# Kernel tuning notes

Measured on AMD Instinct MI355X. Metric: run time of the kernel, lower is better.

## Reference

```python
import jax, jax.numpy as jnp
import numpy as np

TEMPERATURE = 0.5
EPS = 1e-20


def setup_inputs() -> dict:
    key = jax.random.key(0)
    ks = jax.random.split(key, 7)
    N, T, S = 16, 64, 1024
    SRC, TGT, D = 512, 512, 64
    return {
        "input": jax.random.normal(ks[0], (N, T, TGT), jnp.float32),
        "memory_bank": jax.random.normal(ks[1], (N, S, SRC), jnp.float32),
        "W_q": jax.random.normal(ks[2], (TGT, D), jnp.float32) / np.sqrt(TGT),
        "W_ctx": jax.random.normal(ks[3], (SRC, D), jnp.float32) / np.sqrt(SRC),
        "v": jax.random.normal(ks[4], (D,), jnp.float32) / np.sqrt(D),
        "W_out": jax.random.normal(ks[5], (SRC + TGT, TGT), jnp.float32) / np.sqrt(SRC + TGT),
        "b_out": jax.random.normal(ks[6], (TGT,), jnp.float32) * 0.01,
    }


def reference(input, memory_bank, W_q, W_ctx, v, W_out, b_out):
    # MLP attention score: v^T tanh(W_q q + W_ctx h)
    wq = jnp.einsum("ntd,de->nte", input, W_q)            # [N,T,D]
    uh = jnp.einsum("nsd,de->nse", memory_bank, W_ctx)    # [N,S,D]
    wquh = jnp.tanh(wq[:, :, None, :] + uh[:, None, :, :])  # [N,T,S,D]
    scores = jnp.einsum("ntsd,d->nts", wquh, v)           # [N,T,S]

    log_alpha = jax.nn.log_softmax(scores, axis=-1)
    alpha = jnp.exp(log_alpha)                            # c_align_vectors

    # deterministic context + output
    context_c = jnp.einsum("nts,nsd->ntd", alpha, memory_bank)
    h_c = jnp.tanh(jnp.concatenate([input, context_c], axis=-1) @ W_out + b_out)

    # gumbel-softmax sample (K = n_samples = 1, forced by view_as in original)
    u = jax.random.uniform(jax.random.key(42), log_alpha.shape, jnp.float32)
    g = -jnp.log(-jnp.log(u + EPS) + EPS)                 # gumbel noise
    y_align = jax.nn.softmax((log_alpha + g) / TEMPERATURE, axis=-1)  # [N,T,S]

    context_y = jnp.einsum("nts,nsd->ntd", y_align, memory_bank)
    h_y = jnp.tanh(jnp.concatenate([input, context_y], axis=-1) @ W_out + b_out)

    return jnp.stack([h_c, h_y], axis=0)  # [2,N,T,tgt_dim]
```

## Files before the change

kernel.cpp:

```cpp
#include <hip/hip_runtime.h>
#include <hip/hip_bf16.h>
#include <stdint.h>

#define DEV __device__ __forceinline__

typedef __attribute__((ext_vector_type(8))) short short8;
typedef __attribute__((ext_vector_type(4))) float f32x4;

#define TWO_LOG2E 2.8853900817779268f

DEV unsigned short f2bf(float f) {
  uint32_t u = __float_as_uint(f);
  u += 0x7FFFu + ((u >> 16) & 1u);
  return (unsigned short)(u >> 16);
}

DEV uint2 pk4(float4 f) {
  union { __hip_bfloat162 h; unsigned u; } a, b;
  a.h = __float22bfloat162_rn(make_float2(f.x, f.y));
  b.h = __float22bfloat162_rn(make_float2(f.z, f.w));
  return make_uint2(a.u, b.u);
}

DEV short8 mk8(uint2 lo, uint2 hi) {
  union { short8 s; uint4 u; } t;
  t.u = make_uint4(lo.x, lo.y, hi.x, hi.y);
  return t.s;
}

DEV uint32_t rotl32(uint32_t x, int r) { return (x << r) | (x >> (32 - r)); }

DEV void threefry_0_42(uint32_t x0, uint32_t x1, uint32_t& o0, uint32_t& o1) {
  const uint32_t ks0 = 0u, ks1 = 42u, ks2 = 0x1BD11BDAu ^ 42u;
  x0 += ks0; x1 += ks1;
#define TFR(r) { x0 += x1; x1 = rotl32(x1, (r)); x1 ^= x0; }
  TFR(13) TFR(15) TFR(26) TFR(6)  x0 += ks1; x1 += ks2 + 1u;
  TFR(17) TFR(29) TFR(16) TFR(24) x0 += ks2; x1 += ks0 + 2u;
  TFR(13) TFR(15) TFR(26) TFR(6)  x0 += ks0; x1 += ks1 + 3u;
  TFR(17) TFR(29) TFR(16) TFR(24) x0 += ks1; x1 += ks2 + 4u;
  TFR(13) TFR(15) TFR(26) TFR(6)  x0 += ks2; x1 += ks0 + 5u;
#undef TFR
  o0 = x0; o1 = x1;
}

DEV float wredmax(float v) {
#pragma unroll
  for (int off = 32; off > 0; off >>= 1) v = fmaxf(v, __shfl_xor(v, off));
  return v;
}
DEV float wredsum(float v) {
#pragma unroll
  for (int off = 32; off > 0; off >>= 1) v += __shfl_xor(v, off);
  return v;
}

__global__ __launch_bounds__(256) void transpose_all(const float* __restrict__ Wctx,
                                                     const float* __restrict__ Wq,
                                                     const float* __restrict__ Wout,
                                                     unsigned short* __restrict__ WctxT,
                                                     unsigned short* __restrict__ WqT,
                                                     unsigned short* __restrict__ WoutT) {
  __shared__ float tile[64][65];
  const int b = blockIdx.x;
  const float* src; unsigned short* dst; int R, C, br, bc;
  if (b < 8)       { src = Wctx; dst = WctxT; R = 512;  C = 64;  br = b * 64;        bc = 0; }
  else if (b < 16) { src = Wq;   dst = WqT;   R = 512;  C = 64;  br = (b - 8) * 64;  bc = 0; }
  else { int i = b - 16; src = Wout; dst = WoutT; R = 1024; C = 512; br = (i & 15) * 64; bc = (i >> 4) * 64; }
  const int tid = threadIdx.x;
  const int lr = tid >> 4, lc4 = (tid & 15) * 4;
#pragma unroll
  for (int i = 0; i < 4; ++i) {
    float4 v = *(const float4*)(src + (long)(br + lr + i * 16) * C + bc + lc4);
    tile[lr + i * 16][lc4 + 0] = v.x;
    tile[lr + i * 16][lc4 + 1] = v.y;
    tile[lr + i * 16][lc4 + 2] = v.z;
    tile[lr + i * 16][lc4 + 3] = v.w;
  }
  __syncthreads();
#pragma unroll
  for (int i = 0; i < 4; ++i) {
    int crow = lr + i * 16;
    ushort4 o;
    o.x = f2bf(tile[lc4 + 0][crow]);
    o.y = f2bf(tile[lc4 + 1][crow]);
    o.z = f2bf(tile[lc4 + 2][crow]);
    o.w = f2bf(tile[lc4 + 3][crow]);
    *(ushort4*)(dst + (long)(bc + crow) * R + br + lc4) = o;
  }
}

__global__ __launch_bounds__(256) void gemm_uhwq(const float* __restrict__ mb,
                                                 const float* __restrict__ input,
                                                 const unsigned short* __restrict__ WctxT,
                                                 const unsigned short* __restrict__ WqT,
                                                 float* __restrict__ uhT,
                                                 float* __restrict__ wqo) {
  __shared__ unsigned short As[64][32];
  __shared__ unsigned short Bs[64][32];
  const int tid = threadIdx.x;
  const int bx = blockIdx.x;
  const float* A;  const unsigned short* BT;  int mbase;
  if (bx < 256) { A = mb;    BT = WctxT; mbase = bx * 64; }
  else          { A = input; BT = WqT;   mbase = (bx - 256) * 64; }
  const int srow = tid >> 2, kc = tid & 3;
  const int scol = ((kc ^ (srow & 3)) * 8);
  const int wave = tid >> 6, lane = tid & 63;
  const int wm = (wave >> 1) * 32, wn = (wave & 1) * 32;
  const int q = lane >> 4, r = lane & 15;
  const int c0 = ((q ^ (r & 3)) * 8);
  const float* ap = A + (long)(mbase + srow) * 512 + kc * 8;
  const unsigned short* bp = BT + (long)srow * 512 + kc * 8;
  f32x4 acc[2][2];
#pragma unroll
  for (int i = 0; i < 2; ++i)
#pragma unroll
    for (int j = 0; j < 2; ++j) acc[i][j] = (f32x4){0.f, 0.f, 0.f, 0.f};

  float4 fa0 = *(const float4*)(ap);
  float4 fa1 = *(const float4*)(ap + 4);
  uint4 fb = *(const uint4*)(bp);
  for (int k0 = 0; k0 < 512; k0 += 32) {
    uint2 p0 = pk4(fa0), p1 = pk4(fa1);
    *(uint4*)&As[srow][scol] = make_uint4(p0.x, p0.y, p1.x, p1.y);
    *(uint4*)&Bs[srow][scol] = fb;
    __syncthreads();
    if (k0 + 32 < 512) {
      fa0 = *(const float4*)(ap + k0 + 32);
      fa1 = *(const float4*)(ap + k0 + 36);
      fb = *(const uint4*)(bp + k0 + 32);
    }
    short8 a0 = *(const short8*)&As[wm + r][c0];
    short8 a1 = *(const short8*)&As[wm + 16 + r][c0];
    short8 b0 = *(const short8*)&Bs[wn + r][c0];
    short8 b1 = *(const short8*)&Bs[wn + 16 + r][c0];
    acc[0][0] = __builtin_amdgcn_mfma_f32_16x16x32_bf16(a0, b0, acc[0][0], 0, 0, 0);
    acc[0][1] = __builtin_amdgcn_mfma_f32_16x16x32_bf16(a0, b1, acc[0][1], 0, 0, 0);
    acc[1][0] = __builtin_amdgcn_mfma_f32_16x16x32_bf16(a1, b0, acc[1][0], 0, 0, 0);
    acc[1][1] = __builtin_amdgcn_mfma_f32_16x16x32_bf16(a1, b1, acc[1][1], 0, 0, 0);
    __syncthreads();
  }
#pragma unroll
  for (int i2 = 0; i2 < 2; ++i2)
#pragma unroll
    for (int j2 = 0; j2 < 2; ++j2) {
      int gcol = wn + j2 * 16 + r;
      int m = mbase + wm + i2 * 16 + q * 4;
      if (bx < 256) {
        int n = m >> 10, s0 = m & 1023;
        float4 o;
        o.x = acc[i2][j2][0] * TWO_LOG2E;
        o.y = acc[i2][j2][1] * TWO_LOG2E;
        o.z = acc[i2][j2][2] * TWO_LOG2E;
        o.w = acc[i2][j2][3] * TWO_LOG2E;
        *(float4*)(uhT + (long)n * 65536 + (long)gcol * 1024 + s0) = o;
      } else {
#pragma unroll
        for (int reg = 0; reg < 4; ++reg)
          wqo[(long)(m + reg) * 64 + gcol] = acc[i2][j2][reg] * TWO_LOG2E;
      }
    }
}

__global__ __launch_bounds__(256) void gemm_ctx_mfma(const float* __restrict__ alpha,
                                                     const float* __restrict__ yal,
                                                     const float* __restrict__ mb,
                                                     float* __restrict__ ctx) {
  __shared__ unsigned short As[64][32];
  const int tid = threadIdx.x;
  const int vt = blockIdx.x >> 4, n = blockIdx.x & 15;
  const int dbase = blockIdx.y * 32;
  const int srow = tid >> 2, kc = tid & 3;
  const int scol = ((kc ^ (srow & 3)) * 8);
  const int wave = tid >> 6, lane = tid & 63;
  const int wm = (wave >> 1) * 32, wn = (wave & 1) * 16;
  const int q = lane >> 4, r = lane & 15;
  const int c0 = ((q ^ (r & 3)) * 8);
  const float* Abase = (vt == 0 ? alpha : yal) + (long)n * 65536;
  const float* ap = Abase + (long)srow * 1024 + kc * 8;
  const float* bcol = mb + (long)n * 524288 + dbase + wn + r;
  f32x4 acc[2];
  acc[0] = (f32x4){0.f, 0.f, 0.f, 0.f};
  acc[1] = (f32x4){0.f, 0.f, 0.f, 0.f};

  float4 fa0 = *(const float4*)(ap);
  float4 fa1 = *(const float4*)(ap + 4);
  float bv[8];
#pragma unroll
  for (int j = 0; j < 8; ++j) bv[j] = bcol[(long)(q * 8 + j) * 512];

  for (int k0 = 0; k0 < 1024; k0 += 32) {
    uint2 p0 = pk4(fa0), p1 = pk4(fa1);
    *(uint4*)&As[srow][scol] = make_uint4(p0.x, p0.y, p1.x, p1.y);
    __syncthreads();
    float4 blo = make_float4(bv[0], bv[1], bv[2], bv[3]);
    float4 bhi = make_float4(bv[4], bv[5], bv[6], bv[7]);
    short8 b0 = mk8(pk4(blo), pk4(bhi));
    if (k0 + 32 < 1024) {
      fa0 = *(const float4*)(ap + k0 + 32);
      fa1 = *(const float4*)(ap + k0 + 36);
#pragma unroll
      for (int j = 0; j < 8; ++j) bv[j] = bcol[(long)(k0 + 32 + q * 8 + j) * 512];
    }
    short8 a0 = *(const short8*)&As[wm + r][c0];
    short8 a1 = *(const short8*)&As[wm + 16 + r][c0];
    acc[0] = __builtin_amdgcn_mfma_f32_16x16x32_bf16(a0, b0, acc[0], 0, 0, 0);
    acc[1] = __builtin_amdgcn_mfma_f32_16x16x32_bf16(a1, b0, acc[1], 0, 0, 0);
    __syncthreads();
  }
#pragma unroll
  for (int i2 = 0; i2 < 2; ++i2) {
    int gcol = dbase + wn + r;
#pragma unroll
    for (int reg = 0; reg < 4; ++reg) {
      long grow = (long)vt * 1024 + n * 64 + wm + i2 * 16 + q * 4 + reg;
      ctx[grow * 512 + gcol] = acc[i2][reg];
    }
  }
}

__global__ __launch_bounds__(256) void gemm_out_mfma(const float* __restrict__ input,
                                                     const float* __restrict__ ctx,
                                                     const unsigned short* __restrict__ WoutT,
                                                     const float* __restrict__ bout,
                                                     float* __restrict__ out) {
  __shared__ unsigned short As[64][32];
  __shared__ unsigned short Bs[32][32];
  const int tid = threadIdx.x;
  const int mbase = blockIdx.x * 64, nbase = blockIdx.y * 32;
  const int srow = tid >> 2, kc = tid & 3;
  const int scol = ((kc ^ (srow & 3)) * 8);
  const int wave = tid >> 6, lane = tid & 63;
  const int wm = (wave >> 1) * 32, wn = (wave & 1) * 16;
  const int q = lane >> 4, r = lane & 15;
  const int c0 = ((q ^ (r & 3)) * 8);
  const int vv = mbase >> 10, nt = (mbase + srow) & 1023;
  const float* ap_lo = input + (long)nt * 512 + kc * 8;
  const float* ap_hi = ctx + (long)(vv * 1024 + nt) * 512 + kc * 8 - 512;
  const int brow = (tid & 127) >> 2;
  const unsigned short* bp = WoutT + (long)(nbase + brow) * 1024 + kc * 8;
  f32x4 acc[2];
  acc[0] = (f32x4){0.f, 0.f, 0.f, 0.f};
  acc[1] = (f32x4){0.f, 0.f, 0.f, 0.f};

  float4 fa0 = *(const float4*)(ap_lo);
  float4 fa1 = *(const float4*)(ap_lo + 4);
  uint4 fb;
  if (tid < 128) fb = *(const uint4*)(bp);
  for (int k0 = 0; k0 < 1024; k0 += 32) {
    uint2 p0 = pk4(fa0), p1 = pk4(fa1);
    *(uint4*)&As[srow][scol] = make_uint4(p0.x, p0.y, p1.x, p1.y);
    if (tid < 128) *(uint4*)&Bs[brow][(kc ^ (brow & 3)) * 8] = fb;
    __syncthreads();
    int kn = k0 + 32;
    if (kn < 1024) {
      const float* apn = (kn < 512) ? ap_lo : ap_hi;
      fa0 = *(const float4*)(apn + kn);
      fa1 = *(const float4*)(apn + kn + 4);
      if (tid < 128) fb = *(const uint4*)(bp + kn);
    }
    short8 a0 = *(const short8*)&As[wm + r][c0];
    short8 a1 = *(const short8*)&As[wm + 16 + r][c0];
    short8 b0 = *(const short8*)&Bs[wn + r][c0];
    acc[0] = __builtin_amdgcn_mfma_f32_16x16x32_bf16(a0, b0, acc[0], 0, 0, 0);
    acc[1] = __builtin_amdgcn_mfma_f32_16x16x32_bf16(a1, b0, acc[1], 0, 0, 0);
    __syncthreads();
  }
#pragma unroll
  for (int i2 = 0; i2 < 2; ++i2) {
    int gcol = nbase + wn + r;
    float bb = bout[gcol];
#pragma unroll
    for (int reg = 0; reg < 4; ++reg) {
      int grow = mbase + wm + i2 * 16 + q * 4 + reg;
      float z = acc[i2][reg] + bb;
      float rc = __builtin_amdgcn_rcpf(1.f + __builtin_amdgcn_exp2f(z * TWO_LOG2E));
      out[(long)grow * 512 + gcol] = fmaf(-2.f, rc, 1.f);
    }
  }
}

__global__ __launch_bounds__(256) void scores_kernel(const float* __restrict__ uhT,
                                                     const float* __restrict__ wq2,
                                                     const float* __restrict__ v,
                                                     float* __restrict__ alpha_g,
                                                     float* __restrict__ y_g) {
  const int tid = threadIdx.x;
  const int nt = blockIdx.x;
  const int n = nt >> 6;
  __shared__ float wvs[64];
  __shared__ float vvs[64];
  __shared__ float red[4];
  if (tid < 64) {
    wvs[tid] = wq2[nt * 64 + tid];
    vvs[tid] = v[tid];
  }
  __syncthreads();

  float sumv = 0.f;
#pragma unroll
  for (int d = 0; d < 64; d += 4) {
    float4 vv = *(const float4*)&vvs[d];
    sumv += vv.x + vv.y + vv.z + vv.w;
  }

  const float* un = uhT + (long)n * 65536 + tid * 4;
  float4 racc = make_float4(0.f, 0.f, 0.f, 0.f);
  for (int db = 0; db < 64; db += 8) {
    float4 ub[8];
#pragma unroll
    for (int j = 0; j < 8; ++j) ub[j] = *(const float4*)(un + (long)(db + j) * 1024);
#pragma unroll
    for (int j = 0; j < 8; ++j) {
      float w = wvs[db + j], vvj = vvs[db + j];
      racc.x = fmaf(vvj, __builtin_amdgcn_rcpf(1.f + __builtin_amdgcn_exp2f(ub[j].x + w)), racc.x);
      racc.y = fmaf(vvj, __builtin_amdgcn_rcpf(1.f + __builtin_amdgcn_exp2f(ub[j].y + w)), racc.y);
      racc.z = fmaf(vvj, __builtin_amdgcn_rcpf(1.f + __builtin_amdgcn_exp2f(ub[j].z + w)), racc.z);
      racc.w = fmaf(vvj, __builtin_amdgcn_rcpf(1.f + __builtin_amdgcn_exp2f(ub[j].w + w)), racc.w);
    }
  }
  float lsc[4];
  lsc[0] = fmaf(-2.f, racc.x, sumv);
  lsc[1] = fmaf(-2.f, racc.y, sumv);
  lsc[2] = fmaf(-2.f, racc.z, sumv);
  lsc[3] = fmaf(-2.f, racc.w, sumv);

  const int wv = tid >> 6, ln = tid & 63;
  float m = fmaxf(fmaxf(lsc[0], lsc[1]), fmaxf(lsc[2], lsc[3]));
  m = wredmax(m);
  if (ln == 0) red[wv] = m;
  __syncthreads();
  m = fmaxf(fmaxf(red[0], red[1]), fmaxf(red[2], red[3]));
  __syncthreads();
  float ss = 0.f;
#pragma unroll
  for (int i = 0; i < 4; ++i) ss += __expf(lsc[i] - m);
  ss = wredsum(ss);
  if (ln == 0) red[wv] = ss;
  __syncthreads();
  ss = red[0] + red[1] + red[2] + red[3];
  const float logl = __logf(ss);
  __syncthreads();

  const uint32_t jbase = (uint32_t)nt * 1024u + (uint32_t)tid * 4u;
  float ys[4];
  float4 av;
#pragma unroll
  for (int i = 0; i < 4; ++i) {
    float la = lsc[i] - m - logl;
    ((float*)&av)[i] = __expf(la);
    uint32_t o0, o1;
    threefry_0_42(0u, jbase + i, o0, o1);
    uint32_t bits = o0 ^ o1;
    float u = __uint_as_float((bits >> 9) | 0x3f800000u) - 1.0f;
    float g = -__logf(-__logf(u + 1e-20f) + 1e-20f);
    ys[i] = (la + g) * 2.0f;
  }
  *(float4*)(alpha_g + (long)nt * 1024 + tid * 4) = av;

  float m2 = fmaxf(fmaxf(ys[0], ys[1]), fmaxf(ys[2], ys[3]));
  m2 = wredmax(m2);
  if (ln == 0) red[wv] = m2;
  __syncthreads();
  m2 = fmaxf(fmaxf(red[0], red[1]), fmaxf(red[2], red[3]));
  __syncthreads();
  float s2 = 0.f;
  float4 ye;
#pragma unroll
  for (int i = 0; i < 4; ++i) { ((float*)&ye)[i] = __expf(ys[i] - m2); s2 += ((float*)&ye)[i]; }
  s2 = wredsum(s2);
  if (ln == 0) red[wv] = s2;
  __syncthreads();
  s2 = red[0] + red[1] + red[2] + red[3];
  const float rinv = __fdividef(1.f, s2);
  ye.x *= rinv; ye.y *= rinv; ye.z *= rinv; ye.w *= rinv;
  *(float4*)(y_g + (long)nt * 1024 + tid * 4) = ye;
}

extern "C" void kernel_launch(void* const* d_in, const int* in_sizes, int n_in,
                              void* d_out, int out_size, void* d_ws, size_t ws_size,
                              hipStream_t stream) {
  const float* input = (const float*)d_in[0];
  const float* mb    = (const float*)d_in[1];
  const float* W_q   = (const float*)d_in[2];
  const float* W_ctx = (const float*)d_in[3];
  const float* v     = (const float*)d_in[4];
  const float* W_out = (const float*)d_in[5];
  const float* b_out = (const float*)d_in[6];
  float* out = (float*)d_out;
  float* ws = (float*)d_ws;

  float* uhT   = ws;
  float* wq    = ws + 1048576;
  float* yal   = ws + 1114112;
  unsigned short* WctxT = (unsigned short*)(ws + 2162688);
  unsigned short* WqT   = (unsigned short*)(ws + 2179072);
  unsigned short* WoutT = (unsigned short*)(ws + 2195456);
  float* alpha = out;
  float* ctx   = uhT;

  transpose_all<<<144, 256, 0, stream>>>(W_ctx, W_q, W_out, WctxT, WqT, WoutT);
  gemm_uhwq<<<272, 256, 0, stream>>>(mb, input, WctxT, WqT, uhT, wq);
  scores_kernel<<<1024, 256, 0, stream>>>(uhT, wq, v, alpha, yal);
  gemm_ctx_mfma<<<dim3(32, 16), 256, 0, stream>>>(alpha, yal, mb, ctx);
  gemm_out_mfma<<<dim3(32, 16), 256, 0, stream>>>(input, ctx, WoutT, b_out, out);
}
```

Baseline: 154.3 us.

## Split output GEMM into shared input part, store alpha/y/ctx as bf16, merge ctx blocks

The input half of the concatenated output projection is the same for both the deterministic and the sampled branch. It is now computed once into P, and the output GEMM only runs over the context half, starting from P. Alpha, the Gumbel weights and the context are written as bf16 instead of fp32, which halves intermediate traffic and removes the in-loop conversions. The context GEMM now uses 512-thread blocks that process alpha and y together, so each memory_bank tile is loaded once for both. This adds a launch and a P buffer and takes some precision loss from rounding the context to bf16.

```diff
diff --git a/kernel.cpp b/kernel.cpp
--- a/kernel.cpp
+++ b/kernel.cpp
@@ -161,68 +161,10 @@
     }
 }
 
-__global__ __launch_bounds__(256) void gemm_ctx_mfma(const float* __restrict__ alpha,
-                                                     const float* __restrict__ yal,
-                                                     const float* __restrict__ mb,
-                                                     float* __restrict__ ctx) {
-  __shared__ unsigned short As[64][32];
-  const int tid = threadIdx.x;
-  const int vt = blockIdx.x >> 4, n = blockIdx.x & 15;
-  const int dbase = blockIdx.y * 32;
-  const int srow = tid >> 2, kc = tid & 3;
-  const int scol = ((kc ^ (srow & 3)) * 8);
-  const int wave = tid >> 6, lane = tid & 63;
-  const int wm = (wave >> 1) * 32, wn = (wave & 1) * 16;
-  const int q = lane >> 4, r = lane & 15;
-  const int c0 = ((q ^ (r & 3)) * 8);
-  const float* Abase = (vt == 0 ? alpha : yal) + (long)n * 65536;
-  const float* ap = Abase + (long)srow * 1024 + kc * 8;
-  const float* bcol = mb + (long)n * 524288 + dbase + wn + r;
-  f32x4 acc[2];
-  acc[0] = (f32x4){0.f, 0.f, 0.f, 0.f};
-  acc[1] = (f32x4){0.f, 0.f, 0.f, 0.f};
-
-  float4 fa0 = *(const float4*)(ap);
-  float4 fa1 = *(const float4*)(ap + 4);
-  float bv[8];
-#pragma unroll
-  for (int j = 0; j < 8; ++j) bv[j] = bcol[(long)(q * 8 + j) * 512];
-
-  for (int k0 = 0; k0 < 1024; k0 += 32) {
-    uint2 p0 = pk4(fa0), p1 = pk4(fa1);
-    *(uint4*)&As[srow][scol] = make_uint4(p0.x, p0.y, p1.x, p1.y);
-    __syncthreads();
-    float4 blo = make_float4(bv[0], bv[1], bv[2], bv[3]);
-    float4 bhi = make_float4(bv[4], bv[5], bv[6], bv[7]);
-    short8 b0 = mk8(pk4(blo), pk4(bhi));
-    if (k0 + 32 < 1024) {
-      fa0 = *(const float4*)(ap + k0 + 32);
-      fa1 = *(const float4*)(ap + k0 + 36);
-#pragma unroll
-      for (int j = 0; j < 8; ++j) bv[j] = bcol[(long)(k0 + 32 + q * 8 + j) * 512];
-    }
-    short8 a0 = *(const short8*)&As[wm + r][c0];
-    short8 a1 = *(const short8*)&As[wm + 16 + r][c0];
-    acc[0] = __builtin_amdgcn_mfma_f32_16x16x32_bf16(a0, b0, acc[0], 0, 0, 0);
-    acc[1] = __builtin_amdgcn_mfma_f32_16x16x32_bf16(a1, b0, acc[1], 0, 0, 0);
-    __syncthreads();
-  }
-#pragma unroll
-  for (int i2 = 0; i2 < 2; ++i2) {
-    int gcol = dbase + wn + r;
-#pragma unroll
-    for (int reg = 0; reg < 4; ++reg) {
-      long grow = (long)vt * 1024 + n * 64 + wm + i2 * 16 + q * 4 + reg;
-      ctx[grow * 512 + gcol] = acc[i2][reg];
-    }
-  }
-}
-
-__global__ __launch_bounds__(256) void gemm_out_mfma(const float* __restrict__ input,
-                                                     const float* __restrict__ ctx,
-                                                     const unsigned short* __restrict__ WoutT,
-                                                     const float* __restrict__ bout,
-                                                     float* __restrict__ out) {
+__global__ __launch_bounds__(256) void gemm_pre(const float* __restrict__ input,
+                                                const unsigned short* __restrict__ WoutT,
+                                                const float* __restrict__ bout,
+                                                float* __restrict__ P) {
   __shared__ unsigned short As[64][32];
   __shared__ unsigned short Bs[32][32];
   const int tid = threadIdx.x;
@@ -233,29 +175,26 @@
   const int wm = (wave >> 1) * 32, wn = (wave & 1) * 16;
   const int q = lane >> 4, r = lane & 15;
   const int c0 = ((q ^ (r & 3)) * 8);
-  const int vv = mbase >> 10, nt = (mbase + srow) & 1023;
-  const float* ap_lo = input + (long)nt * 512 + kc * 8;
-  const float* ap_hi = ctx + (long)(vv * 1024 + nt) * 512 + kc * 8 - 512;
+  const float* ap = input + (long)(mbase + srow) * 512 + kc * 8;
   const int brow = (tid & 127) >> 2;
   const unsigned short* bp = WoutT + (long)(nbase + brow) * 1024 + kc * 8;
   f32x4 acc[2];
   acc[0] = (f32x4){0.f, 0.f, 0.f, 0.f};
   acc[1] = (f32x4){0.f, 0.f, 0.f, 0.f};
 
-  float4 fa0 = *(const float4*)(ap_lo);
-  float4 fa1 = *(const float4*)(ap_lo + 4);
+  float4 fa0 = *(const float4*)(ap);
+  float4 fa1 = *(const float4*)(ap + 4);
   uint4 fb;
   if (tid < 128) fb = *(const uint4*)(bp);
-  for (int k0 = 0; k0 < 1024; k0 += 32) {
+  for (int k0 = 0; k0 < 512; k0 += 32) {
     uint2 p0 = pk4(fa0), p1 = pk4(fa1);
     *(uint4*)&As[srow][scol] = make_uint4(p0.x, p0.y, p1.x, p1.y);
     if (tid < 128) *(uint4*)&Bs[brow][(kc ^ (brow & 3)) * 8] = fb;
     __syncthreads();
     int kn = k0 + 32;
-    if (kn < 1024) {
-      const float* apn = (kn < 512) ? ap_lo : ap_hi;
-      fa0 = *(const float4*)(apn + kn);
-      fa1 = *(const float4*)(apn + kn + 4);
+    if (kn < 512) {
+      fa0 = *(const float4*)(ap + kn);
+      fa1 = *(const float4*)(ap + kn + 4);
       if (tid < 128) fb = *(const uint4*)(bp + kn);
     }
     short8 a0 = *(const short8*)&As[wm + r][c0];
@@ -272,7 +211,118 @@
 #pragma unroll
     for (int reg = 0; reg < 4; ++reg) {
       int grow = mbase + wm + i2 * 16 + q * 4 + reg;
-      float z = acc[i2][reg] + bb;
+      P[(long)grow * 512 + gcol] = acc[i2][reg] + bb;
+    }
+  }
+}
+
+__global__ __launch_bounds__(512) void gemm_ctx_mfma(const unsigned short* __restrict__ alpha,
+                                                     const unsigned short* __restrict__ yal,
+                                                     const float* __restrict__ mb,
+                                                     unsigned short* __restrict__ ctx) {
+  __shared__ unsigned short As[2][64][32];
+  const int tid = threadIdx.x;
+  const int n = blockIdx.x, dbase = blockIdx.y * 32;
+  const int half = tid >> 8, st = tid & 255;
+  const int srow = st >> 2, kc = st & 3;
+  const int scol = ((kc ^ (srow & 3)) * 8);
+  const unsigned short* Ab = (half ? yal : alpha) + (long)n * 65536 + (long)srow * 1024 + kc * 8;
+  const int wave = tid >> 6, lane = tid & 63;
+  const int vt = wave >> 2, wm = ((wave >> 1) & 1) * 32, wn = (wave & 1) * 16;
+  const int q = lane >> 4, r = lane & 15;
+  const int c0 = ((q ^ (r & 3)) * 8);
+  const float* bcol = mb + (long)n * 524288 + dbase + wn + r;
+  f32x4 acc[2];
+  acc[0] = (f32x4){0.f, 0.f, 0.f, 0.f};
+  acc[1] = (f32x4){0.f, 0.f, 0.f, 0.f};
+
+  uint4 fa = *(const uint4*)(Ab);
+  float bv[8];
+#pragma unroll
+  for (int j = 0; j < 8; ++j) bv[j] = bcol[(long)(q * 8 + j) * 512];
+
+  for (int k0 = 0; k0 < 1024; k0 += 32) {
+    *(uint4*)&As[half][srow][scol] = fa;
+    __syncthreads();
+    float4 blo = make_float4(bv[0], bv[1], bv[2], bv[3]);
+    float4 bhi = make_float4(bv[4], bv[5], bv[6], bv[7]);
+    short8 b0 = mk8(pk4(blo), pk4(bhi));
+    if (k0 + 32 < 1024) {
+      fa = *(const uint4*)(Ab + k0 + 32);
+#pragma unroll
+      for (int j = 0; j < 8; ++j) bv[j] = bcol[(long)(k0 + 32 + q * 8 + j) * 512];
+    }
+    short8 a0 = *(const short8*)&As[vt][wm + r][c0];
+    short8 a1 = *(const short8*)&As[vt][wm + 16 + r][c0];
+    acc[0] = __builtin_amdgcn_mfma_f32_16x16x32_bf16(a0, b0, acc[0], 0, 0, 0);
+    acc[1] = __builtin_amdgcn_mfma_f32_16x16x32_bf16(a1, b0, acc[1], 0, 0, 0);
+    __syncthreads();
+  }
+#pragma unroll
+  for (int i2 = 0; i2 < 2; ++i2) {
+    int gcol = dbase + wn + r;
+#pragma unroll
+    for (int reg = 0; reg < 4; ++reg) {
+      long grow = (long)vt * 1024 + n * 64 + wm + i2 * 16 + q * 4 + reg;
+      ctx[grow * 512 + gcol] = f2bf(acc[i2][reg]);
+    }
+  }
+}
+
+__global__ __launch_bounds__(256) void gemm_out_mfma(const unsigned short* __restrict__ ctx,
+                                                     const unsigned short* __restrict__ WoutT,
+                                                     const float* __restrict__ P,
+                                                     float* __restrict__ out) {
+  __shared__ unsigned short As[64][32];
+  __shared__ unsigned short Bs[32][32];
+  const int tid = threadIdx.x;
+  const int mbase = blockIdx.x * 64, nbase = blockIdx.y * 32;
+  const int srow = tid >> 2, kc = tid & 3;
+  const int scol = ((kc ^ (srow & 3)) * 8);
+  const int wave = tid >> 6, lane = tid & 63;
+  const int wm = (wave >> 1) * 32, wn = (wave & 1) * 16;
+  const int q = lane >> 4, r = lane & 15;
+  const int c0 = ((q ^ (r & 3)) * 8);
+  const unsigned short* ap = ctx + (long)(mbase + srow) * 512 + kc * 8;
+  const int brow = (tid & 127) >> 2;
+  const unsigned short* bp = WoutT + (long)(nbase + brow) * 1024 + 512 + kc * 8;
+  f32x4 acc[2];
+#pragma unroll
+  for (int i2 = 0; i2 < 2; ++i2) {
+    int pcol = nbase + wn + r;
+#pragma unroll
+    for (int reg = 0; reg < 4; ++reg) {
+      int prow = (mbase + wm + i2 * 16 + q * 4 + reg) & 1023;
+      acc[i2][reg] = P[(long)prow * 512 + pcol];
+    }
+  }
+
+  uint4 fa = *(const uint4*)(ap);
+  uint4 fb;
+  if (tid < 128) fb = *(const uint4*)(bp);
+  for (int k0 = 0; k0 < 512; k0 += 32) {
+    *(uint4*)&As[srow][scol] = fa;
+    if (tid < 128) *(uint4*)&Bs[brow][(kc ^ (brow & 3)) * 8] = fb;
+    __syncthreads();
+    int kn = k0 + 32;
+    if (kn < 512) {
+      fa = *(const uint4*)(ap + kn);
+      if (tid < 128) fb = *(const uint4*)(bp + kn);
+    }
+    short8 a0 = *(const short8*)&As[wm + r][c0];
+    short8 a1 = *(const short8*)&As[wm + 16 + r][c0];
+    short8 b0 = *(const short8*)&Bs[wn + r][c0];
+    acc[0] = __builtin_amdgcn_mfma_f32_16x16x32_bf16(a0, b0, acc[0], 0, 0, 0);
+    acc[1] = __builtin_amdgcn_mfma_f32_16x16x32_bf16(a1, b0, acc[1], 0, 0, 0);
+    __syncthreads();
+  }
+#pragma unroll
+  for (int i2 = 0; i2 < 2; ++i2) {
+    int gcol = nbase + wn + r;
+#pragma unroll
+    for (int reg = 0; reg < 4; ++reg) {
+      int grow = mbase + wm + i2 * 16 + q * 4 + reg;
+      float z = acc[i2][reg];
       float rc = __builtin_amdgcn_rcpf(1.f + __builtin_amdgcn_exp2f(z * TWO_LOG2E));
       out[(long)grow * 512 + gcol] = fmaf(-2.f, rc, 1.f);
     }
@@ -282,8 +332,8 @@
 __global__ __launch_bounds__(256) void scores_kernel(const float* __restrict__ uhT,
                                                      const float* __restrict__ wq2,
                                                      const float* __restrict__ v,
-                                                     float* __restrict__ alpha_g,
-                                                     float* __restrict__ y_g) {
+                                                     unsigned short* __restrict__ alpha_g,
+                                                     unsigned short* __restrict__ y_g) {
   const int tid = threadIdx.x;
   const int nt = blockIdx.x;
   const int n = nt >> 6;
@@ -355,7 +405,10 @@
     float g = -__logf(-__logf(u + 1e-20f) + 1e-20f);
     ys[i] = (la + g) * 2.0f;
   }
-  *(float4*)(alpha_g + (long)nt * 1024 + tid * 4) = av;
+  {
+    uint2 pa = pk4(av);
+    *(uint2*)(alpha_g + (long)nt * 1024 + tid * 4) = pa;
+  }
 
   float m2 = fmaxf(fmaxf(ys[0], ys[1]), fmaxf(ys[2], ys[3]));
   m2 = wredmax(m2);
@@ -373,7 +426,10 @@
   s2 = red[0] + red[1] + red[2] + red[3];
   const float rinv = __fdividef(1.f, s2);
   ye.x *= rinv; ye.y *= rinv; ye.z *= rinv; ye.w *= rinv;
-  *(float4*)(y_g + (long)nt * 1024 + tid * 4) = ye;
+  {
+    uint2 py = pk4(ye);
+    *(uint2*)(y_g + (long)nt * 1024 + tid * 4) = py;
+  }
 }
 
 extern "C" void kernel_launch(void* const* d_in, const int* in_sizes, int n_in,
@@ -391,16 +447,18 @@
 
   float* uhT   = ws;
   float* wq    = ws + 1048576;
-  float* yal   = ws + 1114112;
+  unsigned short* alpha_bf = (unsigned short*)(ws + 1114112);
+  unsigned short* yal_bf   = (unsigned short*)(ws + 1638400);
   unsigned short* WctxT = (unsigned short*)(ws + 2162688);
   unsigned short* WqT   = (unsigned short*)(ws + 2179072);
   unsigned short* WoutT = (unsigned short*)(ws + 2195456);
-  float* alpha = out;
-  float* ctx   = uhT;
+  unsigned short* ctxb  = (unsigned short*)(ws + 2457600);
+  float* P = ws + 2981888;
 
   transpose_all<<<144, 256, 0, stream>>>(W_ctx, W_q, W_out, WctxT, WqT, WoutT);
   gemm_uhwq<<<272, 256, 0, stream>>>(mb, input, WctxT, WqT, uhT, wq);
-  scores_kernel<<<1024, 256, 0, stream>>>(uhT, wq, v, alpha, yal);
-  gemm_ctx_mfma<<<dim3(32, 16), 256, 0, stream>>>(alpha, yal, mb, ctx);
-  gemm_out_mfma<<<dim3(32, 16), 256, 0, stream>>>(input, ctx, WoutT, b_out, out);
-}
+  gemm_pre<<<dim3(16, 16), 256, 0, stream>>>(input, WoutT, b_out, P);
+  scores_kernel<<<1024, 256, 0, stream>>>(uhT, wq, v, alpha_bf, yal_bf);
+  gemm_ctx_mfma<<<dim3(16, 16), 512, 0, stream>>>(alpha_bf, yal_bf, mb, ctxb);
+  gemm_out_mfma<<<dim3(32, 16), 256, 0, stream>>>(ctxb, WoutT, P, out);
+}
```

Result: no change. 156.7 us (+1.5%).
